# Performance work log

Hardware: AMD Instinct MI355X
Metric: run time of the kernel (lower is better)

The kernel has to match this reference:

```python
import jax, jax.numpy as jnp
import numpy as np

N = 100_000      # nodes
E = 500_000      # bonds
DN = 128         # dim_node_embedding
DB = 64          # dim_bond_embedding
NTOK = 4         # num_bond_token
DIN = 2 * DN + 2 * DB  # 384
LEAKY = 0.001
LN_EPS = 1e-5
DIST_MAX = 20.0
STEP = 0.5


def _lrelu(v):
    return jnp.where(v >= 0, v, LEAKY * v)


def _layernorm(v, w, b):
    m = v.mean(-1, keepdims=True)
    var = ((v - m) ** 2).mean(-1, keepdims=True)
    return (v - m) / jnp.sqrt(var + LN_EPS) * w + b


def setup_inputs() -> dict:
    key = jax.random.key(0)
    ks = jax.random.split(key, 20)
    x = jax.random.normal(ks[0], (N, 3), dtype=jnp.float32) * 3.0
    pos = jax.random.normal(ks[1], (N, 3), dtype=jnp.float32)
    node_embedding = jax.random.normal(ks[2], (N, DN), dtype=jnp.float32)
    i0 = jax.random.randint(ks[3], (E,), 0, N)
    off = jax.random.randint(ks[4], (E,), 1, N)  # nonzero -> no self-bonds
    bond_index = jnp.stack([i0, (i0 + off) % N], axis=1).astype(jnp.int32)
    bond_types = jax.random.randint(ks[5], (E,), 0, NTOK).astype(jnp.int32)
    s = 0.02
    params = dict(
        bond_emb=jax.random.normal(ks[6], (NTOK, DB), dtype=jnp.float32),
        W0=jax.random.normal(ks[7], (DIN, DN), dtype=jnp.float32) * s,
        b0=jnp.zeros((DN,), jnp.float32),
        W1=jax.random.normal(ks[8], (DN, DN), dtype=jnp.float32) * s,
        b1=jnp.zeros((DN,), jnp.float32),
        ln1_w=jnp.ones((DN,), jnp.float32),
        ln1_b=jnp.zeros((DN,), jnp.float32),
        W2=jax.random.normal(ks[9], (DN, DN), dtype=jnp.float32) * s,
        b2=jnp.zeros((DN,), jnp.float32),
        ln2_w=jnp.ones((DN,), jnp.float32),
        ln2_b=jnp.zeros((DN,), jnp.float32),
        Wo=jax.random.normal(ks[10], (DN, 2), dtype=jnp.float32) * s,
        bo=jnp.zeros((2,), jnp.float32),
    )
    return dict(x=x, pos=pos, node_embedding=node_embedding,
                bond_index=bond_index, bond_types=bond_types, **params)


def reference(x, pos, node_embedding, bond_index, bond_types,
              bond_emb, W0, b0, W1, b1, ln1_w, ln1_b,
              W2, b2, ln2_w, ln2_b, Wo, bo):
    i = bond_index[:, 0]
    j = bond_index[:, 1]

    # ---- BondLength geometry ----
    diff = x[i] - x[j]                                   # [E,3]
    dist = jnp.linalg.norm(diff, axis=-1, keepdims=True)  # [E,1]
    u = diff / dist                                       # [E,3] unit j->i? (i-j)/d
    direction = jnp.stack([u, -u], axis=-1)               # [E,3,2]

    # ---- Smearing (gaussian RBF + overflow bin, normalized) ----
    offset = jnp.linspace(0.0, DIST_MAX, DB - 1, dtype=jnp.float32)  # [63]
    delta = DIST_MAX / (DB - 2)
    coeff = -0.5 / (delta * delta)
    rbf = jnp.exp(coeff * (dist - offset) ** 2)            # [E,63]
    ovf = (dist >= DIST_MAX).astype(x.dtype)               # [E,1]
    smear = jnp.concatenate([rbf, ovf], axis=-1)           # [E,64]
    smear = smear / smear.sum(axis=-1, keepdims=True)

    # ---- Edge MLP (LeakyMLP, num_layer=2, dim_end=2) ----
    feat = jnp.concatenate(
        [node_embedding[i], node_embedding[j], bond_emb[bond_types], smear],
        axis=-1)                                           # [E,384]
    h = _lrelu(feat @ W0 + b0)
    h = _lrelu(_layernorm(h @ W1 + b1, ln1_w, ln1_b))
    h = _lrelu(_layernorm(h @ W2 + b2, ln2_w, ln2_b))
    force = h @ Wo + bo                                    # [E,2]

    # ---- position update (scatter-add) ----
    update = force[:, None, :] * direction                 # [E,3,2]
    pos = pos.at[i].add(STEP * update[..., 0])
    pos = pos.at[j].add(STEP * update[..., 1])
    return pos
```

## Files before the change

kernel.cpp:

```cpp
#include <hip/hip_runtime.h>
#include <stdint.h>

#define N_EDGES 500000
#define N_NODES 100000
#define PREP_NG 2

typedef __attribute__((ext_vector_type(8))) short short8;
typedef __attribute__((ext_vector_type(4))) float floatx4;

__device__ __forceinline__ uint16_t f2bf(float f) {
  union { float f; uint32_t u; } cv; cv.f = f;
  uint32_t u = cv.u;
  return (uint16_t)((u + 0x7FFFu + ((u >> 16) & 1u)) >> 16);
}
__device__ __forceinline__ uint32_t pk2bf(float lo, float hi) {
  return __builtin_amdgcn_perm(__float_as_uint(hi), __float_as_uint(lo), 0x07060302u);
}
__device__ __forceinline__ uint16_t bftrunc(float f) {
  return (uint16_t)(__float_as_uint(f) >> 16);
}
__device__ __forceinline__ float bfup(uint16_t h) {
  return __uint_as_float(((uint32_t)h) << 16);
}
__device__ __forceinline__ float bf2f_lo(uint32_t u) {
  return __uint_as_float(u << 16);
}
__device__ __forceinline__ float bf2f_hi(uint32_t u) {
  return __uint_as_float(u & 0xFFFF0000u);
}
__device__ __forceinline__ float lrelu(float v) { return fmaxf(v, 0.001f * v); }

__global__ void prep0_kernel(const float* __restrict__ W0, const float* __restrict__ b0,
                             const float* __restrict__ W1, const float* __restrict__ W2,
                             const float* __restrict__ bemb,
                             uint16_t* __restrict__ w0ab, uint16_t* __restrict__ w0c,
                             uint16_t* __restrict__ w1f, uint16_t* __restrict__ w2f,
                             float* __restrict__ be0f,
                             const float* __restrict__ pos, float* __restrict__ out, int npos) {
  int id = blockIdx.x * 256 + threadIdx.x;
  if (id < 32768) {
    int f = id;
    int j = f & 7, lane = (f >> 3) & 63, ntt = (f >> 9) & 15, ks = f >> 13;
    int k = ks * 32 + (lane >> 4) * 8 + j;
    int row = (ntt < 8) ? k : (128 + k);
    int col = (ntt & 7) * 16 + (lane & 15);
    w0ab[f] = f2bf(W0[row * 128 + col]);
  } else if (id < 40960) {
    int f = id - 32768;
    int j = f & 7, lane = (f >> 3) & 63, nt = (f >> 9) & 7, ks = f >> 12;
    int k = ks * 32 + (lane >> 4) * 8 + j;
    w0c[f] = f2bf(W0[(320 + k) * 128 + nt * 16 + (lane & 15)]);
  } else if (id < 57344) {
    int f = id - 40960;
    int j = f & 7, lane = (f >> 3) & 63, nt = (f >> 9) & 7, ks = f >> 12;
    int k = ks * 32 + (lane >> 4) * 8 + j;
    w1f[f] = f2bf(W1[k * 128 + nt * 16 + (lane & 15)]);
  } else if (id < 73728) {
    int f = id - 57344;
    int j = f & 7, lane = (f >> 3) & 63, nt = (f >> 9) & 7, ks = f >> 12;
    int k = ks * 32 + (lane >> 4) * 8 + j;
    w2f[f] = f2bf(W2[k * 128 + nt * 16 + (lane & 15)]);
  } else if (id < 74240) {
    int t = id - 73728; int ty = t >> 7, n = t & 127;
    float s = b0[n];
    for (int kk = 0; kk < 64; ++kk) s += bemb[ty * 64 + kk] * W0[(256 + kk) * 128 + n];
    be0f[t] = s;
  } else if (id - 74240 < npos) {
    out[id - 74240] = pos[id - 74240];
  }
}

__global__ __attribute__((amdgpu_flat_work_group_size(256, 256), amdgpu_waves_per_eu(1, 4)))
void prep_p_kernel(const float* __restrict__ nemb, const uint16_t* __restrict__ w0ab,
                   uint16_t* __restrict__ Pa, uint16_t* __restrict__ Pb) {
  __shared__ __align__(16) uint16_t aLds[4 * PREP_NG * 16 * 136];
  const int tid = threadIdx.x;
  const int lane = tid & 63;
  const int wave = tid >> 6;
  const int n15 = lane & 15;
  const int quad = lane >> 4;
  uint16_t* myA = aLds + wave * (PREP_NG * 16 * 136);
  const int base = blockIdx.x * (64 * PREP_NG) + wave * (16 * PREP_NG);

  {
    const int le = lane >> 2, sub = lane & 3;
#pragma unroll
    for (int it = 0; it < PREP_NG; ++it) {
      int r = base + it * 16 + le; if (r >= N_NODES) r = N_NODES - 1;
      const float4* src = (const float4*)(nemb + (size_t)r * 128);
#pragma unroll
      for (int g = 0; g < 4; ++g) {
        float4 a = src[sub * 8 + g * 2], b = src[sub * 8 + g * 2 + 1];
        uint4 pk;
        pk.x = pk2bf(a.x, a.y); pk.y = pk2bf(a.z, a.w);
        pk.z = pk2bf(b.x, b.y); pk.w = pk2bf(b.z, b.w);
        *(uint4*)(myA + (it * 16 + le) * 136 + sub * 32 + g * 8) = pk;
      }
    }
  }

  const short8* wfv = (const short8*)w0ab + lane;
#pragma unroll
  for (int q = 0; q < 4; ++q) {
    short8 bfr[16];
#pragma unroll
    for (int ks = 0; ks < 4; ++ks)
#pragma unroll
      for (int nq = 0; nq < 4; ++nq)
        bfr[ks * 4 + nq] = wfv[(ks * 16 + q * 4 + nq) * 64];
#pragma unroll
    for (int it = 0; it < PREP_NG; ++it) {
      floatx4 acc[4];
#pragma unroll
      for (int nq = 0; nq < 4; ++nq) acc[nq] = (floatx4){0.f, 0.f, 0.f, 0.f};
#pragma unroll
      for (int ks = 0; ks < 4; ++ks) {
        short8 a = *(const short8*)(myA + (it * 16 + n15) * 136 + ks * 32 + quad * 8);
#pragma unroll
        for (int nq = 0; nq < 4; ++nq)
          acc[nq] = __builtin_amdgcn_mfma_f32_16x16x32_bf16(a, bfr[ks * 4 + nq], acc[nq], 0, 0, 0);
      }
      uint16_t* dst = (q < 2) ? Pa : Pb;
      int cbase = ((q & 1) * 4) * 16 + n15;
#pragma unroll
      for (int nq = 0; nq < 4; ++nq) {
        int c = cbase + nq * 16;
#pragma unroll
        for (int r = 0; r < 4; ++r) {
          int row = base + it * 16 + quad * 4 + r;
          if (row < N_NODES) dst[(size_t)row * 128 + c] = bftrunc(acc[nq][r]);
        }
      }
    }
  }
}

template <int NKS>
__device__ __forceinline__ void gemm_fw(const uint16_t* __restrict__ wf,
                                        const uint16_t* aRow, int lane, floatx4* acc) {
  const short8* wfv = (const short8*)wf + lane;
  short8 a[NKS];
#pragma unroll
  for (int ks = 0; ks < NKS; ++ks) a[ks] = *(const short8*)(aRow + ks * 32);
#pragma unroll
  for (int ks = 0; ks < NKS; ++ks) {
#pragma unroll
    for (int nt = 0; nt < 8; ++nt) {
      short8 b = wfv[(ks * 8 + nt) * 64];
      acc[nt] = __builtin_amdgcn_mfma_f32_16x16x32_bf16(a[ks], b, acc[nt], 0, 0, 0);
    }
  }
}

__global__ __attribute__((amdgpu_flat_work_group_size(256, 256)))
void bond_mlp_kernel(const float* __restrict__ x,
                     const int* __restrict__ bidx, const int* __restrict__ btyp,
                     const uint16_t* __restrict__ Pa, const uint16_t* __restrict__ Pb,
                     const uint16_t* __restrict__ w0c, const uint16_t* __restrict__ w1f,
                     const uint16_t* __restrict__ w2f, const float* __restrict__ be0f,
                     const float* __restrict__ b1, const float* __restrict__ ln1w,
                     const float* __restrict__ ln1b,
                     const float* __restrict__ b2, const float* __restrict__ ln2w,
                     const float* __restrict__ ln2b,
                     const float* __restrict__ Wo, const float* __restrict__ bo,
                     float* __restrict__ out) {
  __shared__ __align__(16) uint16_t wlds[4 * 3328];
  __shared__ float u_lds[64][3];
  __shared__ int ij_lds[64][2];
  __shared__ int type_lds[64];

  const int tid = threadIdx.x;
  const int lane = tid & 63;
  const int wave = tid >> 6;
  const int n15 = lane & 15;
  const int quad = lane >> 4;

  uint16_t* hA = wlds + wave * 3328;
  uint16_t* smearA = hA + 2176;

  {
    const int le = lane >> 2, sub = lane & 3;
    const int lrow = le;
    const int ge = blockIdx.x * 64 + wave * 16 + le;
    const bool valid = ge < N_EDGES;
    int vi = 0, vj = 0, bt = 0;
    if (valid) { vi = bidx[2 * ge]; vj = bidx[2 * ge + 1]; bt = btyp[ge]; }
    float dx, dy, dz;
    if (valid) {
      dx = x[3 * vi]     - x[3 * vj];
      dy = x[3 * vi + 1] - x[3 * vj + 1];
      dz = x[3 * vi + 2] - x[3 * vj + 2];
    } else { dx = 1.0f; dy = 0.0f; dz = 0.0f; }
    float dist = sqrtf(dx * dx + dy * dy + dz * dz);
    float rinv = 1.0f / dist;
    if (sub == 0) {
      int gr = wave * 16 + lrow;
      u_lds[gr][0] = dx * rinv; u_lds[gr][1] = dy * rinv; u_lds[gr][2] = dz * rinv;
      ij_lds[gr][0] = vi; ij_lds[gr][1] = vj; type_lds[gr] = bt;
    }
    const uint4* pa = (const uint4*)(Pa + (size_t)vi * 128);
    const uint4* pb = (const uint4*)(Pb + (size_t)vj * 128);
    const float4* bbp = (const float4*)(be0f + bt * 128);
#pragma unroll
    for (int g = 0; g < 4; ++g) {
      uint4 av = pa[sub * 4 + g];
      uint4 bv = pb[sub * 4 + g];
      float4 e0 = bbp[sub * 8 + g * 2], e1 = bbp[sub * 8 + g * 2 + 1];
      uint4 pk;
      pk.x = pk2bf(bf2f_lo(av.x) + bf2f_lo(bv.x) + e0.x,
                   bf2f_hi(av.x) + bf2f_hi(bv.x) + e0.y);
      pk.y = pk2bf(bf2f_lo(av.y) + bf2f_lo(bv.y) + e0.z,
                   bf2f_hi(av.y) + bf2f_hi(bv.y) + e0.w);
      pk.z = pk2bf(bf2f_lo(av.z) + bf2f_lo(bv.z) + e1.x,
                   bf2f_hi(av.z) + bf2f_hi(bv.z) + e1.y);
      pk.w = pk2bf(bf2f_lo(av.w) + bf2f_lo(bv.w) + e1.z,
                   bf2f_hi(av.w) + bf2f_hi(bv.w) + e1.w);
      *(uint4*)(hA + lrow * 136 + sub * 32 + g * 8) = pk;
    }
    const float delta = 20.0f / 62.0f;
    const float coeff = -0.5f / (delta * delta);
    float sv[16]; float ssum = 0.0f;
#pragma unroll
    for (int t = 0; t < 16; ++t) {
      int kk = sub * 16 + t;
      float v;
      if (kk < 63) { float d = dist - (float)kk * delta; v = __expf(coeff * d * d); }
      else v = (dist >= 20.0f) ? 1.0f : 0.0f;
      sv[t] = v; ssum += v;
    }
    ssum += __shfl_xor(ssum, 1);
    ssum += __shfl_xor(ssum, 2);
    float sinv = 1.0f / ssum;
#pragma unroll
    for (int g = 0; g < 2; ++g) {
      uint4 pk;
      pk.x = pk2bf(sv[g*8+0]*sinv, sv[g*8+1]*sinv);
      pk.y = pk2bf(sv[g*8+2]*sinv, sv[g*8+3]*sinv);
      pk.z = pk2bf(sv[g*8+4]*sinv, sv[g*8+5]*sinv);
      pk.w = pk2bf(sv[g*8+6]*sinv, sv[g*8+7]*sinv);
      *(uint4*)(smearA + lrow * 72 + sub * 16 + g * 8) = pk;
    }
  }

  floatx4 acc[8];
#pragma unroll
  for (int nt = 0; nt < 8; ++nt)
#pragma unroll
    for (int r = 0; r < 4; ++r)
      acc[nt][r] = bfup(hA[(quad * 4 + r) * 136 + nt * 16 + n15]);

  gemm_fw<2>(w0c, smearA + n15 * 72 + quad * 8, lane, acc);

#pragma unroll
  for (int nt = 0; nt < 8; ++nt)
#pragma unroll
    for (int r = 0; r < 4; ++r)
      hA[(quad * 4 + r) * 136 + nt * 16 + n15] = bftrunc(lrelu(acc[nt][r]));

#pragma unroll
  for (int nt = 0; nt < 8; ++nt) acc[nt] = (floatx4){0.f, 0.f, 0.f, 0.f};
  gemm_fw<4>(w1f, hA + n15 * 136 + quad * 8, lane, acc);

  {
    float bv[8], wv[8], bb2[8];
#pragma unroll
    for (int nt = 0; nt < 8; ++nt) {
      int col = nt * 16 + n15;
      bv[nt] = b1[col]; wv[nt] = ln1w[col]; bb2[nt] = ln1b[col];
    }
    float s[4] = {0,0,0,0}, q[4] = {0,0,0,0};
#pragma unroll
    for (int nt = 0; nt < 8; ++nt)
#pragma unroll
      for (int r = 0; r < 4; ++r) { float v = acc[nt][r] + bv[nt]; s[r] += v; q[r] += v * v; }
#pragma unroll
    for (int m = 1; m <= 8; m <<= 1)
#pragma unroll
      for (int r = 0; r < 4; ++r) { s[r] += __shfl_xor(s[r], m); q[r] += __shfl_xor(q[r], m); }
    float mean[4], rstd[4];
#pragma unroll
    for (int r = 0; r < 4; ++r) {
      mean[r] = s[r] * (1.0f / 128.0f);
      float var = q[r] * (1.0f / 128.0f) - mean[r] * mean[r];
      rstd[r] = rsqrtf(var + 1e-5f);
    }
#pragma unroll
    for (int nt = 0; nt < 8; ++nt)
#pragma unroll
      for (int r = 0; r < 4; ++r) {
        float v = acc[nt][r] + bv[nt];
        float vn = (v - mean[r]) * rstd[r] * wv[nt] + bb2[nt];
        hA[(quad * 4 + r) * 136 + nt * 16 + n15] = bftrunc(lrelu(vn));
      }
  }

#pragma unroll
  for (int nt = 0; nt < 8; ++nt) acc[nt] = (floatx4){0.f, 0.f, 0.f, 0.f};
  gemm_fw<4>(w2f, hA + n15 * 136 + quad * 8, lane, acc);

  {
    float bv[8], wv[8], bb2[8], wo0[8], wo1[8];
#pragma unroll
    for (int nt = 0; nt < 8; ++nt) {
      int col = nt * 16 + n15;
      bv[nt] = b2[col]; wv[nt] = ln2w[col]; bb2[nt] = ln2b[col];
      wo0[nt] = Wo[2 * col]; wo1[nt] = Wo[2 * col + 1];
    }
    float s[4] = {0,0,0,0}, q[4] = {0,0,0,0};
#pragma unroll
    for (int nt = 0; nt < 8; ++nt)
#pragma unroll
      for (int r = 0; r < 4; ++r) { float v = acc[nt][r] + bv[nt]; s[r] += v; q[r] += v * v; }
#pragma unroll
    for (int m = 1; m <= 8; m <<= 1)
#pragma unroll
      for (int r = 0; r < 4; ++r) { s[r] += __shfl_xor(s[r], m); q[r] += __shfl_xor(q[r], m); }
    float mean[4], rstd[4];
#pragma unroll
    for (int r = 0; r < 4; ++r) {
      mean[r] = s[r] * (1.0f / 128.0f);
      float var = q[r] * (1.0f / 128.0f) - mean[r] * mean[r];
      rstd[r] = rsqrtf(var + 1e-5f);
    }
    float f0[4] = {0,0,0,0}, f1[4] = {0,0,0,0};
#pragma unroll
    for (int nt = 0; nt < 8; ++nt)
#pragma unroll
      for (int r = 0; r < 4; ++r) {
        float v = acc[nt][r] + bv[nt];
        float vn = lrelu((v - mean[r]) * rstd[r] * wv[nt] + bb2[nt]);
        f0[r] += vn * wo0[nt];
        f1[r] += vn * wo1[nt];
      }
#pragma unroll
    for (int m = 1; m <= 8; m <<= 1)
#pragma unroll
      for (int r = 0; r < 4; ++r) { f0[r] += __shfl_xor(f0[r], m); f1[r] += __shfl_xor(f1[r], m); }

    if (n15 < 4) {
      int gr = wave * 16 + quad * 4 + n15;
      int ge2 = blockIdx.x * 64 + gr;
      if (ge2 < N_EDGES) {
        float F0 = (n15 == 0) ? f0[0] : (n15 == 1) ? f0[1] : (n15 == 2) ? f0[2] : f0[3];
        float F1 = (n15 == 0) ? f1[0] : (n15 == 1) ? f1[1] : (n15 == 2) ? f1[2] : f1[3];
        F0 += bo[0]; F1 += bo[1];
        float ux = u_lds[gr][0], uy = u_lds[gr][1], uz = u_lds[gr][2];
        int ii = ij_lds[gr][0], jj = ij_lds[gr][1];
        float c0 = 0.5f * F0;
        float c1 = -0.5f * F1;
        atomicAdd(out + 3 * ii,     c0 * ux);
        atomicAdd(out + 3 * ii + 1, c0 * uy);
        atomicAdd(out + 3 * ii + 2, c0 * uz);
        atomicAdd(out + 3 * jj,     c1 * ux);
        atomicAdd(out + 3 * jj + 1, c1 * uy);
        atomicAdd(out + 3 * jj + 2, c1 * uz);
      }
    }
  }
}

extern "C" void kernel_launch(void* const* d_in, const int* in_sizes, int n_in,
                              void* d_out, int out_size, void* d_ws, size_t ws_size,
                              hipStream_t stream) {
  const float* x    = (const float*)d_in[0];
  const float* pos  = (const float*)d_in[1];
  const float* nemb = (const float*)d_in[2];
  const int*   bidx = (const int*)d_in[3];
  const int*   btyp = (const int*)d_in[4];
  const float* bemb = (const float*)d_in[5];
  const float* W0   = (const float*)d_in[6];
  const float* b0   = (const float*)d_in[7];
  const float* W1   = (const float*)d_in[8];
  const float* b1   = (const float*)d_in[9];
  const float* ln1w = (const float*)d_in[10];
  const float* ln1b = (const float*)d_in[11];
  const float* W2   = (const float*)d_in[12];
  const float* b2   = (const float*)d_in[13];
  const float* ln2w = (const float*)d_in[14];
  const float* ln2b = (const float*)d_in[15];
  const float* Wo   = (const float*)d_in[16];
  const float* bo   = (const float*)d_in[17];
  float* out = (float*)d_out;

  uint16_t* w0ab = (uint16_t*)d_ws;
  uint16_t* w0c  = w0ab + 32768;
  uint16_t* w1f  = w0c + 8192;
  uint16_t* w2f  = w1f + 16384;
  float*    be0f = (float*)(w2f + 16384);
  uint16_t* Pa   = (uint16_t*)(be0f + 512);
  uint16_t* Pb   = Pa + (size_t)N_NODES * 128;

  prep0_kernel<<<(74240 + out_size + 255) / 256, 256, 0, stream>>>(
      W0, b0, W1, W2, bemb, w0ab, w0c, w1f, w2f, be0f, pos, out, out_size);
  prep_p_kernel<<<(N_NODES + 64 * PREP_NG - 1) / (64 * PREP_NG), 256, 0, stream>>>(
      nemb, w0ab, Pa, Pb);
  bond_mlp_kernel<<<(N_EDGES + 63) / 64, 256, 0, stream>>>(
      x, bidx, btyp, Pa, Pb, w0c, w1f, w2f, be0f,
      b1, ln1w, ln1b, b2, ln2w, ln2b, Wo, bo, out);
}
```

Baseline: 353.7 us.

## Tabulate smearing projection by distance and type, process two row tiles per wave

Replaces the per-bond Gaussian smearing and its 64-wide GEMM with a precomputed bf16 table of (bond-type bias + normalized smear @ W0) over distance bins, linearly interpolated per bond. Each wave now handles 32 bonds as two 16-row tiles sharing weight fragment loads in the W1/W2 MFMA loops. This removes exp work and one MFMA stage per bond and amortizes weight loads, at the cost of an extra table-build kernel, interpolation error versus exact RBF, and higher register pressure.

Measured after the change: 407.6 us. +15.2%, slower.

```diff
diff --git a/kernel.cpp b/kernel.cpp
--- a/kernel.cpp
+++ b/kernel.cpp
@@ -4,6 +4,7 @@
 #define N_EDGES 500000
 #define N_NODES 100000
 #define PREP_NG 2
+#define TBINS 1280
 
 typedef __attribute__((ext_vector_type(8))) short short8;
 typedef __attribute__((ext_vector_type(4))) float floatx4;
@@ -19,23 +20,15 @@
 __device__ __forceinline__ uint16_t bftrunc(float f) {
   return (uint16_t)(__float_as_uint(f) >> 16);
 }
-__device__ __forceinline__ float bfup(uint16_t h) {
-  return __uint_as_float(((uint32_t)h) << 16);
-}
-__device__ __forceinline__ float bf2f_lo(uint32_t u) {
-  return __uint_as_float(u << 16);
-}
-__device__ __forceinline__ float bf2f_hi(uint32_t u) {
-  return __uint_as_float(u & 0xFFFF0000u);
-}
+__device__ __forceinline__ float bf2f_lo(uint32_t u) { return __uint_as_float(u << 16); }
+__device__ __forceinline__ float bf2f_hi(uint32_t u) { return __uint_as_float(u & 0xFFFF0000u); }
 __device__ __forceinline__ float lrelu(float v) { return fmaxf(v, 0.001f * v); }
 
 __global__ void prep0_kernel(const float* __restrict__ W0, const float* __restrict__ b0,
                              const float* __restrict__ W1, const float* __restrict__ W2,
                              const float* __restrict__ bemb,
-                             uint16_t* __restrict__ w0ab, uint16_t* __restrict__ w0c,
-                             uint16_t* __restrict__ w1f, uint16_t* __restrict__ w2f,
-                             float* __restrict__ be0f,
+                             uint16_t* __restrict__ w0ab, uint16_t* __restrict__ w1f,
+                             uint16_t* __restrict__ w2f, float* __restrict__ be0f,
                              const float* __restrict__ pos, float* __restrict__ out, int npos) {
   int id = blockIdx.x * 256 + threadIdx.x;
   if (id < 32768) {
@@ -45,29 +38,49 @@
     int row = (ntt < 8) ? k : (128 + k);
     int col = (ntt & 7) * 16 + (lane & 15);
     w0ab[f] = f2bf(W0[row * 128 + col]);
-  } else if (id < 40960) {
+  } else if (id < 49152) {
     int f = id - 32768;
     int j = f & 7, lane = (f >> 3) & 63, nt = (f >> 9) & 7, ks = f >> 12;
     int k = ks * 32 + (lane >> 4) * 8 + j;
-    w0c[f] = f2bf(W0[(320 + k) * 128 + nt * 16 + (lane & 15)]);
-  } else if (id < 57344) {
-    int f = id - 40960;
-    int j = f & 7, lane = (f >> 3) & 63, nt = (f >> 9) & 7, ks = f >> 12;
-    int k = ks * 32 + (lane >> 4) * 8 + j;
     w1f[f] = f2bf(W1[k * 128 + nt * 16 + (lane & 15)]);
-  } else if (id < 73728) {
-    int f = id - 57344;
+  } else if (id < 65536) {
+    int f = id - 49152;
     int j = f & 7, lane = (f >> 3) & 63, nt = (f >> 9) & 7, ks = f >> 12;
     int k = ks * 32 + (lane >> 4) * 8 + j;
     w2f[f] = f2bf(W2[k * 128 + nt * 16 + (lane & 15)]);
-  } else if (id < 74240) {
-    int t = id - 73728; int ty = t >> 7, n = t & 127;
+  } else if (id < 66048) {
+    int t = id - 65536; int ty = t >> 7, n = t & 127;
     float s = b0[n];
     for (int kk = 0; kk < 64; ++kk) s += bemb[ty * 64 + kk] * W0[(256 + kk) * 128 + n];
     be0f[t] = s;
-  } else if (id - 74240 < npos) {
-    out[id - 74240] = pos[id - 74240];
-  }
+  } else if (id - 66048 < npos) {
+    out[id - 66048] = pos[id - 66048];
+  }
+}
+
+__global__ void prep_t_kernel(const float* __restrict__ W0, const float* __restrict__ be0f,
+                              uint16_t* __restrict__ T) {
+  int id = blockIdx.x * 256 + threadIdx.x;
+  if (id >= 4 * TBINS * 128) return;
+  int n = id & 127;
+  int tb = id >> 7;
+  int b = tb % TBINS;
+  int ty = tb / TBINS;
+  float dist = (float)b * (1.0f / 32.0f);
+  const float delta = 20.0f / 62.0f;
+  const float coeff = -0.5f / (delta * delta);
+  float sum = 0.0f;
+  for (int k = 0; k < 63; ++k) { float d = dist - (float)k * delta; sum += __expf(coeff * d * d); }
+  float ovf = (dist >= 20.0f) ? 1.0f : 0.0f;
+  sum += ovf;
+  float rs = 1.0f / sum;
+  float s = be0f[ty * 128 + n];
+  for (int k = 0; k < 63; ++k) {
+    float d = dist - (float)k * delta;
+    s += __expf(coeff * d * d) * rs * W0[(320 + k) * 128 + n];
+  }
+  s += ovf * rs * W0[(320 + 63) * 128 + n];
+  T[id] = f2bf(s);
 }
 
 __global__ __attribute__((amdgpu_flat_work_group_size(256, 256), amdgpu_waves_per_eu(1, 4)))
@@ -136,38 +149,41 @@
 }
 
 template <int NKS>
-__device__ __forceinline__ void gemm_fw(const uint16_t* __restrict__ wf,
-                                        const uint16_t* aRow, int lane, floatx4* acc) {
+__device__ __forceinline__ void gemm2(const uint16_t* __restrict__ wf,
+                                      const uint16_t* aR0, const uint16_t* aR1,
+                                      int lane, floatx4* acc0, floatx4* acc1) {
   const short8* wfv = (const short8*)wf + lane;
-  short8 a[NKS];
-#pragma unroll
-  for (int ks = 0; ks < NKS; ++ks) a[ks] = *(const short8*)(aRow + ks * 32);
+  short8 a0[NKS], a1[NKS];
 #pragma unroll
   for (int ks = 0; ks < NKS; ++ks) {
+    a0[ks] = *(const short8*)(aR0 + ks * 32);
+    a1[ks] = *(const short8*)(aR1 + ks * 32);
+  }
+#pragma unroll
+  for (int ks = 0; ks < NKS; ++ks)
 #pragma unroll
     for (int nt = 0; nt < 8; ++nt) {
       short8 b = wfv[(ks * 8 + nt) * 64];
-      acc[nt] = __builtin_amdgcn_mfma_f32_16x16x32_bf16(a[ks], b, acc[nt], 0, 0, 0);
-    }
-  }
+      acc0[nt] = __builtin_amdgcn_mfma_f32_16x16x32_bf16(a0[ks], b, acc0[nt], 0, 0, 0);
+      acc1[nt] = __builtin_amdgcn_mfma_f32_16x16x32_bf16(a1[ks], b, acc1[nt], 0, 0, 0);
+    }
 }
 
 __global__ __attribute__((amdgpu_flat_work_group_size(256, 256)))
 void bond_mlp_kernel(const float* __restrict__ x,
                      const int* __restrict__ bidx, const int* __restrict__ btyp,
                      const uint16_t* __restrict__ Pa, const uint16_t* __restrict__ Pb,
-                     const uint16_t* __restrict__ w0c, const uint16_t* __restrict__ w1f,
-                     const uint16_t* __restrict__ w2f, const float* __restrict__ be0f,
+                     const uint16_t* __restrict__ Tt, const uint16_t* __restrict__ w1f,
+                     const uint16_t* __restrict__ w2f,
                      const float* __restrict__ b1, const float* __restrict__ ln1w,
                      const float* __restrict__ ln1b,
                      const float* __restrict__ b2, const float* __restrict__ ln2w,
                      const float* __restrict__ ln2b,
                      const float* __restrict__ Wo, const float* __restrict__ bo,
                      float* __restrict__ out) {
-  __shared__ __align__(16) uint16_t wlds[4 * 3328];
-  __shared__ float u_lds[64][3];
-  __shared__ int ij_lds[64][2];
-  __shared__ int type_lds[64];
+  __shared__ __align__(16) uint16_t hA_all[4 * 32 * 136];
+  __shared__ float u_lds[128][3];
+  __shared__ int ij_lds[128][2];
 
   const int tid = threadIdx.x;
   const int lane = tid & 63;
@@ -175,13 +191,14 @@
   const int n15 = lane & 15;
   const int quad = lane >> 4;
 
-  uint16_t* hA = wlds + wave * 3328;
-  uint16_t* smearA = hA + 2176;
-
-  {
+  uint16_t* hA = hA_all + wave * (32 * 136);
+
+#pragma unroll
+  for (int p = 0; p < 2; ++p) {
     const int le = lane >> 2, sub = lane & 3;
-    const int lrow = le;
-    const int ge = blockIdx.x * 64 + wave * 16 + le;
+    const int row = p * 16 + le;
+    const int gr = wave * 32 + row;
+    const int ge = blockIdx.x * 128 + gr;
     const bool valid = ge < N_EDGES;
     int vi = 0, vj = 0, bt = 0;
     if (valid) { vi = bidx[2 * ge]; vj = bidx[2 * ge + 1]; bt = btyp[ge]; }
@@ -194,72 +211,55 @@
     float dist = sqrtf(dx * dx + dy * dy + dz * dz);
     float rinv = 1.0f / dist;
     if (sub == 0) {
-      int gr = wave * 16 + lrow;
       u_lds[gr][0] = dx * rinv; u_lds[gr][1] = dy * rinv; u_lds[gr][2] = dz * rinv;
-      ij_lds[gr][0] = vi; ij_lds[gr][1] = vj; type_lds[gr] = bt;
-    }
-    const uint4* pa = (const uint4*)(Pa + (size_t)vi * 128);
-    const uint4* pb = (const uint4*)(Pb + (size_t)vj * 128);
-    const float4* bbp = (const float4*)(be0f + bt * 128);
+      ij_lds[gr][0] = vi; ij_lds[gr][1] = vj;
+    }
+    float fb = fminf(dist, 39.5f) * 32.0f;
+    int bi = (int)fb;
+    float w = fb - (float)bi;
+    const uint4* pa = (const uint4*)(Pa + (size_t)vi * 128 + sub * 32);
+    const uint4* pb = (const uint4*)(Pb + (size_t)vj * 128 + sub * 32);
+    const uint16_t* trow = Tt + ((size_t)(bt * TBINS + bi)) * 128 + sub * 32;
+    const uint4* t0p = (const uint4*)trow;
+    const uint4* t1p = (const uint4*)(trow + 128);
 #pragma unroll
     for (int g = 0; g < 4; ++g) {
-      uint4 av = pa[sub * 4 + g];
-      uint4 bv = pb[sub * 4 + g];
-      float4 e0 = bbp[sub * 8 + g * 2], e1 = bbp[sub * 8 + g * 2 + 1];
+      uint4 av = pa[g], bv = pb[g], t0 = t0p[g], t1 = t1p[g];
       uint4 pk;
-      pk.x = pk2bf(bf2f_lo(av.x) + bf2f_lo(bv.x) + e0.x,
-                   bf2f_hi(av.x) + bf2f_hi(bv.x) + e0.y);
-      pk.y = pk2bf(bf2f_lo(av.y) + bf2f_lo(bv.y) + e0.z,
-                   bf2f_hi(av.y) + bf2f_hi(bv.y) + e0.w);
-      pk.z = pk2bf(bf2f_lo(av.z) + bf2f_lo(bv.z) + e1.x,
-                   bf2f_hi(av.z) + bf2f_hi(bv.z) + e1.y);
-      pk.w = pk2bf(bf2f_lo(av.w) + bf2f_lo(bv.w) + e1.z,
-                   bf2f_hi(av.w) + bf2f_hi(bv.w) + e1.w);
-      *(uint4*)(hA + lrow * 136 + sub * 32 + g * 8) = pk;
-    }
-    const float delta = 20.0f / 62.0f;
-    const float coeff = -0.5f / (delta * delta);
-    float sv[16]; float ssum = 0.0f;
-#pragma unroll
-    for (int t = 0; t < 16; ++t) {
-      int kk = sub * 16 + t;
-      float v;
-      if (kk < 63) { float d = dist - (float)kk * delta; v = __expf(coeff * d * d); }
-      else v = (dist >= 20.0f) ? 1.0f : 0.0f;
-      sv[t] = v; ssum += v;
-    }
-    ssum += __shfl_xor(ssum, 1);
-    ssum += __shfl_xor(ssum, 2);
-    float sinv = 1.0f / ssum;
-#pragma unroll
-    for (int g = 0; g < 2; ++g) {
-      uint4 pk;
-      pk.x = pk2bf(sv[g*8+0]*sinv, sv[g*8+1]*sinv);
-      pk.y = pk2bf(sv[g*8+2]*sinv, sv[g*8+3]*sinv);
-      pk.z = pk2bf(sv[g*8+4]*sinv, sv[g*8+5]*sinv);
-      pk.w = pk2bf(sv[g*8+6]*sinv, sv[g*8+7]*sinv);
-      *(uint4*)(smearA + lrow * 72 + sub * 16 + g * 8) = pk;
-    }
-  }
-
-  floatx4 acc[8];
-#pragma unroll
-  for (int nt = 0; nt < 8; ++nt)
-#pragma unroll
-    for (int r = 0; r < 4; ++r)
-      acc[nt][r] = bfup(hA[(quad * 4 + r) * 136 + nt * 16 + n15]);
-
-  gemm_fw<2>(w0c, smearA + n15 * 72 + quad * 8, lane, acc);
-
-#pragma unroll
-  for (int nt = 0; nt < 8; ++nt)
-#pragma unroll
-    for (int r = 0; r < 4; ++r)
-      hA[(quad * 4 + r) * 136 + nt * 16 + n15] = bftrunc(lrelu(acc[nt][r]));
-
-#pragma unroll
-  for (int nt = 0; nt < 8; ++nt) acc[nt] = (floatx4){0.f, 0.f, 0.f, 0.f};
-  gemm_fw<4>(w1f, hA + n15 * 136 + quad * 8, lane, acc);
+      {
+        float lo = bf2f_lo(av.x) + bf2f_lo(bv.x), hi = bf2f_hi(av.x) + bf2f_hi(bv.x);
+        float l0 = bf2f_lo(t0.x), l1 = bf2f_lo(t1.x), h0 = bf2f_hi(t0.x), h1 = bf2f_hi(t1.x);
+        pk.x = pk2bf(lrelu(lo + l0 + w * (l1 - l0)), lrelu(hi + h0 + w * (h1 - h0)));
+      }
+      {
+        float lo = bf2f_lo(av.y) + bf2f_lo(bv.y), hi = bf2f_hi(av.y) + bf2f_hi(bv.y);
+        float l0 = bf2f_lo(t0.y), l1 = bf2f_lo(t1.y), h0 = bf2f_hi(t0.y), h1 = bf2f_hi(t1.y);
+        pk.y = pk2bf(lrelu(lo + l0 + w * (l1 - l0)), lrelu(hi + h0 + w * (h1 - h0)));
+      }
+      {
+        float lo = bf2f_lo(av.z) + bf2f_lo(bv.z), hi = bf2f_hi(av.z) + bf2f_hi(bv.z);
+        float l0 = bf2f_lo(t0.z), l1 = bf2f_lo(t1.z), h0 = bf2f_hi(t0.z), h1 = bf2f_hi(t1.z);
+        pk.z = pk2bf(lrelu(lo + l0 + w * (l1 - l0)), lrelu(hi + h0 + w * (h1 - h0)));
+      }
+      {
+        float lo = bf2f_lo(av.w) + bf2f_lo(bv.w), hi = bf2f_hi(av.w) + bf2f_hi(bv.w);
+        float l0 = bf2f_lo(t0.w), l1 = bf2f_lo(t1.w), h0 = bf2f_hi(t0.w), h1 = bf2f_hi(t1.w);
+        pk.w = pk2bf(lrelu(lo + l0 + w * (l1 - l0)), lrelu(hi + h0 + w * (h1 - h0)));
+      }
+      *(uint4*)(hA + row * 136 + sub * 32 + g * 8) = pk;
+    }
+  }
+
+  const uint16_t* aR0 = hA + n15 * 136 + quad * 8;
+  const uint16_t* aR1 = hA + (16 + n15) * 136 + quad * 8;
+
+  floatx4 acc0[8], acc1[8];
+#pragma unroll
+  for (int nt = 0; nt < 8; ++nt) {
+    acc0[nt] = (floatx4){0.f, 0.f, 0.f, 0.f};
+    acc1[nt] = (floatx4){0.f, 0.f, 0.f, 0.f};
+  }
+  gemm2<4>(w1f, aR0, aR1, lane, acc0, acc1);
 
   {
     float bv[8], wv[8], bb2[8];
@@ -268,35 +268,42 @@
       int col = nt * 16 + n15;
       bv[nt] = b1[col]; wv[nt] = ln1w[col]; bb2[nt] = ln1b[col];
     }
-    float s[4] = {0,0,0,0}, q[4] = {0,0,0,0};
-#pragma unroll
-    for (int nt = 0; nt < 8; ++nt)
-#pragma unroll
-      for (int r = 0; r < 4; ++r) { float v = acc[nt][r] + bv[nt]; s[r] += v; q[r] += v * v; }
-#pragma unroll
-    for (int m = 1; m <= 8; m <<= 1)
-#pragma unroll
-      for (int r = 0; r < 4; ++r) { s[r] += __shfl_xor(s[r], m); q[r] += __shfl_xor(q[r], m); }
-    float mean[4], rstd[4];
-#pragma unroll
-    for (int r = 0; r < 4; ++r) {
-      mean[r] = s[r] * (1.0f / 128.0f);
-      float var = q[r] * (1.0f / 128.0f) - mean[r] * mean[r];
-      rstd[r] = rsqrtf(var + 1e-5f);
-    }
-#pragma unroll
-    for (int nt = 0; nt < 8; ++nt)
+#pragma unroll
+    for (int t = 0; t < 2; ++t) {
+      floatx4* acc = t ? acc1 : acc0;
+      float s[4] = {0,0,0,0}, q[4] = {0,0,0,0};
+#pragma unroll
+      for (int nt = 0; nt < 8; ++nt)
+#pragma unroll
+        for (int r = 0; r < 4; ++r) { float v = acc[nt][r] + bv[nt]; s[r] += v; q[r] += v * v; }
+#pragma unroll
+      for (int m = 1; m <= 8; m <<= 1)
+#pragma unroll
+        for (int r = 0; r < 4; ++r) { s[r] += __shfl_xor(s[r], m); q[r] += __shfl_xor(q[r], m); }
+      float mean[4], rstd[4];
 #pragma unroll
       for (int r = 0; r < 4; ++r) {
-        float v = acc[nt][r] + bv[nt];
-        float vn = (v - mean[r]) * rstd[r] * wv[nt] + bb2[nt];
-        hA[(quad * 4 + r) * 136 + nt * 16 + n15] = bftrunc(lrelu(vn));
-      }
-  }
-
-#pragma unroll
-  for (int nt = 0; nt < 8; ++nt) acc[nt] = (floatx4){0.f, 0.f, 0.f, 0.f};
-  gemm_fw<4>(w2f, hA + n15 * 136 + quad * 8, lane, acc);
+        mean[r] = s[r] * (1.0f / 128.0f);
+        float var = q[r] * (1.0f / 128.0f) - mean[r] * mean[r];
+        rstd[r] = rsqrtf(var + 1e-5f);
+      }
+#pragma unroll
+      for (int nt = 0; nt < 8; ++nt)
+#pragma unroll
+        for (int r = 0; r < 4; ++r) {
+          float v = acc[nt][r] + bv[nt];
+          float vn = (v - mean[r]) * rstd[r] * wv[nt] + bb2[nt];
+          hA[(t * 16 + quad * 4 + r) * 136 + nt * 16 + n15] = bftrunc(lrelu(vn));
+        }
+    }
+  }
+
+#pragma unroll
+  for (int nt = 0; nt < 8; ++nt) {
+    acc0[nt] = (floatx4){0.f, 0.f, 0.f, 0.f};
+    acc1[nt] = (floatx4){0.f, 0.f, 0.f, 0.f};
+  }
+  gemm2<4>(w2f, aR0, aR1, lane, acc0, acc1);
 
   {
     float bv[8], wv[8], bb2[8], wo0[8], wo1[8];
@@ -306,54 +313,59 @@
       bv[nt] = b2[col]; wv[nt] = ln2w[col]; bb2[nt] = ln2b[col];
       wo0[nt] = Wo[2 * col]; wo1[nt] = Wo[2 * col + 1];
     }
-    float s[4] = {0,0,0,0}, q[4] = {0,0,0,0};
-#pragma unroll
-    for (int nt = 0; nt < 8; ++nt)
-#pragma unroll
-      for (int r = 0; r < 4; ++r) { float v = acc[nt][r] + bv[nt]; s[r] += v; q[r] += v * v; }
-#pragma unroll
-    for (int m = 1; m <= 8; m <<= 1)
-#pragma unroll
-      for (int r = 0; r < 4; ++r) { s[r] += __shfl_xor(s[r], m); q[r] += __shfl_xor(q[r], m); }
-    float mean[4], rstd[4];
-#pragma unroll
-    for (int r = 0; r < 4; ++r) {
-      mean[r] = s[r] * (1.0f / 128.0f);
-      float var = q[r] * (1.0f / 128.0f) - mean[r] * mean[r];
-      rstd[r] = rsqrtf(var + 1e-5f);
-    }
-    float f0[4] = {0,0,0,0}, f1[4] = {0,0,0,0};
-#pragma unroll
-    for (int nt = 0; nt < 8; ++nt)
+    float bo0 = bo[0], bo1 = bo[1];
+#pragma unroll
+    for (int t = 0; t < 2; ++t) {
+      floatx4* acc = t ? acc1 : acc0;
+      float s[4] = {0,0,0,0}, q[4] = {0,0,0,0};
+#pragma unroll
+      for (int nt = 0; nt < 8; ++nt)
+#pragma unroll
+        for (int r = 0; r < 4; ++r) { float v = acc[nt][r] + bv[nt]; s[r] += v; q[r] += v * v; }
+#pragma unroll
+      for (int m = 1; m <= 8; m <<= 1)
+#pragma unroll
+        for (int r = 0; r < 4; ++r) { s[r] += __shfl_xor(s[r], m); q[r] += __shfl_xor(q[r], m); }
+      float mean[4], rstd[4];
 #pragma unroll
       for (int r = 0; r < 4; ++r) {
-        float v = acc[nt][r] + bv[nt];
-        float vn = lrelu((v - mean[r]) * rstd[r] * wv[nt] + bb2[nt]);
-        f0[r] += vn * wo0[nt];
-        f1[r] += vn * wo1[nt];
-      }
-#pragma unroll
-    for (int m = 1; m <= 8; m <<= 1)
-#pragma unroll
-      for (int r = 0; r < 4; ++r) { f0[r] += __shfl_xor(f0[r], m); f1[r] += __shfl_xor(f1[r], m); }
-
-    if (n15 < 4) {
-      int gr = wave * 16 + quad * 4 + n15;
-      int ge2 = blockIdx.x * 64 + gr;
-      if (ge2 < N_EDGES) {
-        float F0 = (n15 == 0) ? f0[0] : (n15 == 1) ? f0[1] : (n15 == 2) ? f0[2] : f0[3];
-        float F1 = (n15 == 0) ? f1[0] : (n15 == 1) ? f1[1] : (n15 == 2) ? f1[2] : f1[3];
-        F0 += bo[0]; F1 += bo[1];
-        float ux = u_lds[gr][0], uy = u_lds[gr][1], uz = u_lds[gr][2];
-        int ii = ij_lds[gr][0], jj = ij_lds[gr][1];
-        float c0 = 0.5f * F0;
-        float c1 = -0.5f * F1;
-        atomicAdd(out + 3 * ii,     c0 * ux);
-        atomicAdd(out + 3 * ii + 1, c0 * uy);
-        atomicAdd(out + 3 * ii + 2, c0 * uz);
-        atomicAdd(out + 3 * jj,     c1 * ux);
-        atomicAdd(out + 3 * jj + 1, c1 * uy);
-        atomicAdd(out + 3 * jj + 2, c1 * uz);
+        mean[r] = s[r] * (1.0f / 128.0f);
+        float var = q[r] * (1.0f / 128.0f) - mean[r] * mean[r];
+        rstd[r] = rsqrtf(var + 1e-5f);
+      }
+      float f0[4] = {0,0,0,0}, f1[4] = {0,0,0,0};
+#pragma unroll
+      for (int nt = 0; nt < 8; ++nt)
+#pragma unroll
+        for (int r = 0; r < 4; ++r) {
+          float v = acc[nt][r] + bv[nt];
+          float vn = lrelu((v - mean[r]) * rstd[r] * wv[nt] + bb2[nt]);
+          f0[r] += vn * wo0[nt];
+          f1[r] += vn * wo1[nt];
+        }
+#pragma unroll
+      for (int m = 1; m <= 8; m <<= 1)
+#pragma unroll
+        for (int r = 0; r < 4; ++r) { f0[r] += __shfl_xor(f0[r], m); f1[r] += __shfl_xor(f1[r], m); }
+
+      if (n15 < 4) {
+        int gr = wave * 32 + t * 16 + quad * 4 + n15;
+        int ge2 = blockIdx.x * 128 + gr;
+        if (ge2 < N_EDGES) {
+          float F0 = (n15 == 0) ? f0[0] : (n15 == 1) ? f0[1] : (n15 == 2) ? f0[2] : f0[3];
+          float F1 = (n15 == 0) ? f1[0] : (n15 == 1) ? f1[1] : (n15 == 2) ? f1[2] : f1[3];
+          F0 += bo0; F1 += bo1;
+          float ux = u_lds[gr][0], uy = u_lds[gr][1], uz = u_lds[gr][2];
+          int ii = ij_lds[gr][0], jj = ij_lds[gr][1];
+          float c0 = 0.5f * F0;
+          float c1 = -0.5f * F1;
+          atomicAdd(out + 3 * ii,     c0 * ux);
+          atomicAdd(out + 3 * ii + 1, c0 * uy);
+          atomicAdd(out + 3 * ii + 2, c0 * uz);
+          atomicAdd(out + 3 * jj,     c1 * ux);
+          atomicAdd(out + 3 * jj + 1, c1 * uy);
+          atomicAdd(out + 3 * jj + 2, c1 * uz);
+        }
       }
     }
   }
@@ -383,18 +395,19 @@
   float* out = (float*)d_out;
 
   uint16_t* w0ab = (uint16_t*)d_ws;
-  uint16_t* w0c  = w0ab + 32768;
-  uint16_t* w1f  = w0c + 8192;
+  uint16_t* w1f  = w0ab + 32768;
   uint16_t* w2f  = w1f + 16384;
   float*    be0f = (float*)(w2f + 16384);
-  uint16_t* Pa   = (uint16_t*)(be0f + 512);
+  uint16_t* Tt   = (uint16_t*)(be0f + 512);
+  uint16_t* Pa   = Tt + 4 * TBINS * 128;
   uint16_t* Pb   = Pa + (size_t)N_NODES * 128;
 
-  prep0_kernel<<<(74240 + out_size + 255) / 256, 256, 0, stream>>>(
-      W0, b0, W1, W2, bemb, w0ab, w0c, w1f, w2f, be0f, pos, out, out_size);
+  prep0_kernel<<<(66048 + out_size + 255) / 256, 256, 0, stream>>>(
+      W0, b0, W1, W2, bemb, w0ab, w1f, w2f, be0f, pos, out, out_size);
+  prep_t_kernel<<<(4 * TBINS * 128 + 255) / 256, 256, 0, stream>>>(W0, be0f, Tt);
   prep_p_kernel<<<(N_NODES + 64 * PREP_NG - 1) / (64 * PREP_NG), 256, 0, stream>>>(
       nemb, w0ab, Pa, Pb);
-  bond_mlp_kernel<<<(N_EDGES + 63) / 64, 256, 0, stream>>>(
-      x, bidx, btyp, Pa, Pb, w0c, w1f, w2f, be0f,
+  bond_mlp_kernel<<<(N_EDGES + 127) / 128, 256, 0, stream>>>(
+      x, bidx, btyp, Pa, Pb, Tt, w1f, w2f,
       b1, ln1w, ln1b, b2, ln2w, ln2b, Wo, bo, out);
 }
```
